# Kernel optimization log

Measured on AMD Instinct MI355X. Metric: run time of the kernel, lower is better.

Reference implementation:

```python
import jax, jax.numpy as jnp
import numpy as np

N = 50000      # nodes
E = 800000     # edges (before self-loops)
F_IN = 512     # input features
H = 8          # heads (layer 1)
C = 32         # hidden per head
CLS = 40       # classes


def setup_inputs() -> dict:
    key = jax.random.key(0)
    ks = jax.random.split(key, 10)
    small = lambda k, shape: jax.random.normal(k, shape, jnp.float32) * 0.05
    return {
        "x": jax.random.normal(ks[0], (N, F_IN), jnp.float32),
        "edge_index": jax.random.randint(ks[1], (2, E), 0, N, jnp.int32),
        # layer 1 params (GATConv: F_IN -> C per head, 8 heads, concat)
        "W1": small(ks[2], (F_IN, H * C)),
        "a_src1": small(ks[3], (H, C)),
        "a_dst1": small(ks[4], (H, C)),
        "b1": jnp.zeros((H * C,), jnp.float32),
        # layer 2 params (GATConv: H*C -> CLS, 1 head)
        "W2": small(ks[5], (H * C, CLS)),
        "a_src2": small(ks[6], (1, CLS)),
        "a_dst2": small(ks[7], (1, CLS)),
        "b2": jnp.zeros((CLS,), jnp.float32),
    }


def gat_conv(x, W, a_src, a_dst, b, src, dst, n):
    """PyG-style GATConv (negative_slope=0.2); self-loops already in src/dst."""
    h_, c_ = a_src.shape
    h = (x @ W).reshape(n, h_, c_)                       # [N, H, C]
    alpha_src = jnp.einsum('nhc,hc->nh', h, a_src)       # [N, H]
    alpha_dst = jnp.einsum('nhc,hc->nh', h, a_dst)       # [N, H]
    e = jax.nn.leaky_relu(alpha_src[src] + alpha_dst[dst], 0.2)  # [E', H]
    # segment softmax over incoming edges of each destination node
    m = jax.lax.stop_gradient(jax.ops.segment_max(e, dst, num_segments=n))
    ex = jnp.exp(e - m[dst])
    den = jax.ops.segment_sum(ex, dst, num_segments=n)
    alpha = ex / (den[dst] + 1e-16)                      # [E', H]
    out = jax.ops.segment_sum(h[src] * alpha[:, :, None], dst, num_segments=n)
    return out.reshape(n, h_ * c_) + b


def reference(x, edge_index, W1, a_src1, a_dst1, b1, W2, a_src2, a_dst2, b2):
    n = x.shape[0]
    loop = jnp.arange(n, dtype=edge_index.dtype)
    src = jnp.concatenate([edge_index[0], loop])  # add self-loops (PyG default)
    dst = jnp.concatenate([edge_index[1], loop])
    # dropout is identity at inference
    h = jax.nn.elu(gat_conv(x, W1, a_src1, a_dst1, b1, src, dst, n))
    out = gat_conv(h, W2, a_src2, a_dst2, b2, src, dst, n)
    return jax.nn.log_softmax(out, axis=1)
```

## Files before the change

kernel.cpp:

```cpp
#include <hip/hip_runtime.h>
#include <hip/hip_bf16.h>
#include <math.h>

constexpr int NN  = 50000;
constexpr int NE  = 800000;
constexpr int EP  = NE + NN;
constexpr int FIN = 512;
constexpr int NH  = 8;
constexpr int NC  = 32;
constexpr int HC  = NH * NC;
constexpr int CLS = 40;
constexpr int CLSP = 48;
constexpr int DSTR = 16;
constexpr int NGB  = (NN + 63) / 64;
constexpr int NHB  = (NE + 255) / 256;
constexpr int NFB  = NGB + NHB;
constexpr int NP2B = (EP + 255) / 256;
constexpr int CVTW_ITEMS = HC * (FIN / 8) + CLSP * HC;
constexpr int CVTW_B = (CVTW_ITEMS + 255) / 256;

typedef __attribute__((ext_vector_type(8))) __bf16 bf16x8;
typedef __attribute__((ext_vector_type(4))) __bf16 bf16x4;
typedef __attribute__((ext_vector_type(4))) float f32x4;
typedef __attribute__((ext_vector_type(2))) float f32x2;

__device__ inline bf16x8 cvt8v(const f32x4 a, const f32x4 b) {
  bf16x8 o;
  o[0] = (__bf16)a.x; o[1] = (__bf16)a.y; o[2] = (__bf16)a.z; o[3] = (__bf16)a.w;
  o[4] = (__bf16)b.x; o[5] = (__bf16)b.y; o[6] = (__bf16)b.z; o[7] = (__bf16)b.w;
  return o;
}

__device__ inline unsigned char to_fp8(float f) {
  int pk = __builtin_amdgcn_cvt_pk_fp8_f32(f, f, 0, false);
  return (unsigned char)(pk & 0xff);
}

__device__ inline float from_fp8(unsigned char b) {
  f32x2 v = __builtin_amdgcn_cvt_pk_f32_fp8((unsigned)b, false);
  return v.x;
}

__global__ void k_cvtw(const float* __restrict__ W1, const float* __restrict__ W2,
                       __bf16* __restrict__ Wt, __bf16* __restrict__ W2t) {
  int t = blockIdx.x * 256 + threadIdx.x;
  if (t < HC * (FIN / 8)) {
    int c = t >> 6, kq = (t & 63) * 8;
    bf16x8 o;
#pragma unroll
    for (int j = 0; j < 8; ++j) o[j] = (__bf16)W1[(size_t)(kq + j) * HC + c];
    *(bf16x8*)&Wt[(size_t)c * FIN + kq] = o;
  } else if (t < CVTW_ITEMS) {
    int u = t - HC * (FIN / 8);
    int c = u >> 8, k = u & 255;
    W2t[u] = (c < CLS) ? (__bf16)W2[(size_t)k * CLS + c] : (__bf16)0.f;
  }
}

__global__ __launch_bounds__(256) void k_gemm1_hist(
    const float* __restrict__ X, const __bf16* __restrict__ Wt,
    const float* __restrict__ a_s1, const float* __restrict__ a_d1,
    unsigned char* __restrict__ Hout, float* __restrict__ asrc1,
    float* __restrict__ adst1,
    const int* __restrict__ ei, int* __restrict__ degp,
    int* __restrict__ rank) {
  __shared__ __align__(16) float Xp[2][4096];
  const int tid = threadIdx.x;

  if (blockIdx.x >= NGB) {
    int e = (blockIdx.x - NGB) * 256 + tid;
    if (e < NE) {
      int d = ei[NE + e];
      rank[e] = atomicAdd(&degp[(size_t)d * DSTR], 1);
    }
    return;
  }

  const int lane = tid & 63;
  const int w    = tid >> 6;
  const int wn   = w * 64;
  const int bm   = blockIdx.x * 64;
  const int l15  = lane & 15, lg = lane >> 4;

  const int srow_l  = (lane >> 4);
  const int sslot   = (l15 >> 1);
  const int shalf   = (lane & 1);

  f32x4 acc[4][4] = {};

  auto issue = [&](int c, int buf) {
#pragma unroll
    for (int jj = 0; jj < 4; ++jj) {
      const int j = w * 4 + jj;
      const int row_l = 4 * j + srow_l;
      const int rowG = min(bm + row_l, NN - 1);
      const int g = sslot ^ (row_l & 7);
      const float* src = X + (size_t)rowG * FIN + c * 64 + g * 8 + shalf * 4;
      __builtin_amdgcn_global_load_lds(
          (const __attribute__((address_space(1))) void*)src,
          (__attribute__((address_space(3))) void*)(&Xp[buf][j * 256]), 16, 0, 0);
    }
  };

  issue(0, 0);
  for (int c = 0; c < 8; ++c) {
    const int cur = c & 1;
    __syncthreads();
    if (c < 7) issue(c + 1, cur ^ 1);

#pragma unroll
    for (int kh = 0; kh < 2; ++kh) {
      const int kb = lg + 4 * kh;
      bf16x8 bv[4];
#pragma unroll
      for (int ni = 0; ni < 4; ++ni)
        bv[ni] = *(const bf16x8*)(Wt + (size_t)(wn + ni * 16 + l15) * FIN
                                     + c * 64 + kb * 8);
#pragma unroll
      for (int mi = 0; mi < 4; ++mi) {
        int r = mi * 16 + l15;
        int fo = r * 64 + ((kb ^ (r & 7)) << 3);
        f32x4 alo = *(const f32x4*)&Xp[cur][fo];
        f32x4 ahi = *(const f32x4*)&Xp[cur][fo + 4];
        bf16x8 av = cvt8v(alo, ahi);
#pragma unroll
        for (int ni = 0; ni < 4; ++ni)
          acc[mi][ni] = __builtin_amdgcn_mfma_f32_16x16x32_bf16(
              av, bv[ni], acc[mi][ni], 0, 0, 0);
      }
    }
  }

  const int hbase = 2 * w;
#pragma unroll
  for (int hh = 0; hh < 2; ++hh) {
    float asA = a_s1[(hbase + hh) * NC + l15];
    float asB = a_s1[(hbase + hh) * NC + 16 + l15];
    float adA = a_d1[(hbase + hh) * NC + l15];
    float adB = a_d1[(hbase + hh) * NC + 16 + l15];
    float vs = 0.f, vd = 0.f;
#pragma unroll
    for (int mi = 0; mi < 4; ++mi) {
#pragma unroll
      for (int r = 0; r < 4; ++r) {
        float ps = acc[mi][2 * hh][r] * asA + acc[mi][2 * hh + 1][r] * asB;
        float pd = acc[mi][2 * hh][r] * adA + acc[mi][2 * hh + 1][r] * adB;
#pragma unroll
        for (int off = 1; off < 16; off <<= 1) {
          ps += __shfl_xor(ps, off, 64);
          pd += __shfl_xor(pd, off, 64);
        }
        if (l15 == mi * 4 + r) { vs = ps; vd = pd; }
      }
    }
    int rw = bm + (l15 >> 2) * 16 + lg * 4 + (l15 & 3);
    if (rw < NN) {
      asrc1[(size_t)rw * NH + hbase + hh] = vs;
      adst1[(size_t)rw * NH + hbase + hh] = vd;
    }
  }

#pragma unroll
  for (int mi = 0; mi < 4; ++mi) {
#pragma unroll
    for (int ni = 0; ni < 4; ++ni) {
      int col = wn + ni * 16 + l15;
#pragma unroll
      for (int r = 0; r < 4; ++r) {
        int row = bm + mi * 16 + lg * 4 + r;
        if (row < NN) Hout[(size_t)row * HC + col] = to_fp8(acc[mi][ni][r]);
      }
    }
  }
}

__global__ __launch_bounds__(1024) void k_scan1(const int* __restrict__ degp,
                                                int* __restrict__ rowptr1,
                                                int* __restrict__ bsum, int n) {
  __shared__ int sm[1024];
  int i = blockIdx.x * 1024 + threadIdx.x;
  int v = (i < n) ? degp[(size_t)i * DSTR] + 1 : 0;
  sm[threadIdx.x] = v;
  __syncthreads();
  for (int off = 1; off < 1024; off <<= 1) {
    int t = (threadIdx.x >= off) ? sm[threadIdx.x - off] : 0;
    __syncthreads();
    sm[threadIdx.x] += t;
    __syncthreads();
  }
  if (i < n) rowptr1[i] = sm[threadIdx.x];
  if (threadIdx.x == 1023) bsum[blockIdx.x] = sm[1023];
}

__global__ void k_scan23(int* __restrict__ rowptr, const int* __restrict__ bsum,
                         int nb, int n) {
  __shared__ int off[64];
  if (threadIdx.x < 64) {
    int lane = threadIdx.x;
    int v = (lane < nb) ? bsum[lane] : 0;
#pragma unroll
    for (int o = 1; o < 64; o <<= 1) {
      int t = __shfl_up(v, o);
      if (lane >= o) v += t;
    }
    int ex = __shfl_up(v, 1);
    if (lane == 0) ex = 0;
    off[lane] = ex;
  }
  __syncthreads();
  int i = blockIdx.x * 256 + threadIdx.x;
  if (i == 0) rowptr[0] = 0;
  if (i < n) rowptr[i + 1] += off[i >> 10];
}

__global__ void k_pass2(const int* __restrict__ ei, const int* __restrict__ rank,
                        const int* __restrict__ rowptr,
                        unsigned short* __restrict__ srcS) {
  int e = blockIdx.x * 256 + threadIdx.x;
  if (e >= EP) return;
  if (e < NE) {
    int s = ei[e], d = ei[NE + e];
    srcS[rowptr[d] + rank[e]] = (unsigned short)s;
  } else {
    int d = e - NE;
    srcS[rowptr[d + 1] - 1] = (unsigned short)d;
  }
}

__global__ __launch_bounds__(256) void k_agg1(const unsigned char* __restrict__ h1f8,
                                              const float* __restrict__ asrc,
                                              const float* __restrict__ adst,
                                              const unsigned short* __restrict__ srcS,
                                              const int* __restrict__ rowptr,
                                              const float* __restrict__ b1,
                                              __bf16* __restrict__ helu) {
  int wave = (blockIdx.x * 256 + threadIdx.x) >> 6;
  int lane = threadIdx.x & 63;
  if (wave >= NN) return;
  int lo = rowptr[wave], hi = rowptr[wave + 1];
  int head = lane >> 3;
  int hw   = lane & 7;
  float adstv = adst[wave * NH + head];
  float ad2   = adst[wave * NH + hw];
  float4 acc = {0.f, 0.f, 0.f, 0.f};
  float den = 0.f;

  for (int base = lo; base < hi; base += 64) {
    int cnt = hi - base; if (cnt > 64) cnt = 64;
    int sv = (lane < cnt) ? (int)srcS[base + lane] : 0;
    int j = 0;
    for (; j + 8 <= cnt; j += 8) {
      int se = __shfl(sv, j + head);
      float v = asrc[se * NH + hw] + ad2;
      v = v > 0.f ? v : 0.2f * v;
      float wv = __expf(v);
      int s[8]; unsigned int hv[8];
#pragma unroll
      for (int u = 0; u < 8; ++u) s[u] = __shfl(sv, j + u);
#pragma unroll
      for (int u = 0; u < 8; ++u)
        hv[u] = *(const unsigned int*)&h1f8[(size_t)s[u] * HC + lane * 4];
#pragma unroll
      for (int u = 0; u < 8; ++u) {
        float wu = __shfl(wv, u * 8 + head);
        f32x2 lo2 = __builtin_amdgcn_cvt_pk_f32_fp8(hv[u], false);
        f32x2 hi2 = __builtin_amdgcn_cvt_pk_f32_fp8(hv[u], true);
        acc.x += wu * lo2.x;
        acc.y += wu * lo2.y;
        acc.z += wu * hi2.x;
        acc.w += wu * hi2.y;
        den += wu;
      }
    }
    for (; j < cnt; ++j) {
      int s = __shfl(sv, j);
      float v = asrc[s * NH + head] + adstv;
      v = v > 0.f ? v : 0.2f * v;
      float w = __expf(v);
      unsigned int hv = *(const unsigned int*)&h1f8[(size_t)s * HC + lane * 4];
      f32x2 lo2 = __builtin_amdgcn_cvt_pk_f32_fp8(hv, false);
      f32x2 hi2 = __builtin_amdgcn_cvt_pk_f32_fp8(hv, true);
      acc.x += w * lo2.x;
      acc.y += w * lo2.y;
      acc.z += w * hi2.x;
      acc.w += w * hi2.y;
      den += w;
    }
  }

  float inv = 1.f / (den + 1e-16f);
  float4 bb = *(const float4*)&b1[lane * 4];
  float o[4] = {acc.x * inv + bb.x, acc.y * inv + bb.y,
                acc.z * inv + bb.z, acc.w * inv + bb.w};
  bf16x4 ov;
#pragma unroll
  for (int j2 = 0; j2 < 4; ++j2) {
    float e = o[j2] > 0.f ? o[j2] : expm1f(o[j2]);
    ov[j2] = (__bf16)e;
  }
  *(bf16x4*)&helu[(size_t)wave * HC + lane * 4] = ov;
}

__global__ __launch_bounds__(256) void k_gemm2m(const __bf16* __restrict__ A,
                                                const __bf16* __restrict__ W2t,
                                                const float* __restrict__ a_s2,
                                                const float* __restrict__ a_d2,
                                                unsigned char* __restrict__ h2p,
                                                float* __restrict__ asrc2,
                                                float* __restrict__ adst2) {
  __shared__ __align__(16) __bf16 As[128 * 8 * 8];
  __shared__ __align__(16) __bf16 Bsh[CLSP * 33 * 8];
  const int tid  = threadIdx.x;
  const int lane = tid & 63;
  const int w    = tid >> 6;
  const int wm   = w * 32;
  const int bm   = blockIdx.x * 128;

  const int l3 = lane >> 3;
  const int l7 = lane & 7;
  const int kb_src = l7 ^ l3;

  for (int s = tid; s < CLSP * 32; s += 256) {
    int c = s >> 5, kb = s & 31;
    *(bf16x8*)(Bsh + (size_t)(c * 33 + kb) * 8) =
        *(const bf16x8*)(W2t + (size_t)c * HC + kb * 8);
  }

  f32x4 acc[2][3] = {};

  for (int step = 0; step < 4; ++step) {
    const int k0 = step * 64;
#pragma unroll
    for (int q = 0; q < 4; ++q) {
      const int inst = w * 4 + q;
      const int r = inst * 8 + l3;
      const int arow = min(bm + r, NN - 1);
      const __bf16* ga = A + (size_t)arow * HC + k0 + kb_src * 8;
      __builtin_amdgcn_global_load_lds(
          (const __attribute__((address_space(1))) void*)ga,
          (__attribute__((address_space(3))) void*)(As + inst * 512), 16, 0, 0);
    }
    __syncthreads();

    const int l15 = lane & 15, lg = lane >> 4;
#pragma unroll
    for (int kh = 0; kh < 2; ++kh) {
      const int kbl = lg + 4 * kh;
      const int kbg = step * 8 + kbl;
      bf16x8 av[2], bv[3];
#pragma unroll
      for (int mi = 0; mi < 2; ++mi) {
        int r = wm + mi * 16 + l15;
        av[mi] = *(const bf16x8*)(As + (size_t)(r * 8 + (kbl ^ (r & 7))) * 8);
      }
#pragma unroll
      for (int ni = 0; ni < 3; ++ni) {
        int c = ni * 16 + l15;
        bv[ni] = *(const bf16x8*)(Bsh + (size_t)(c * 33 + kbg) * 8);
      }
#pragma unroll
      for (int mi = 0; mi < 2; ++mi)
#pragma unroll
        for (int ni = 0; ni < 3; ++ni)
          acc[mi][ni] = __builtin_amdgcn_mfma_f32_16x16x32_bf16(
              av[mi], bv[ni], acc[mi][ni], 0, 0, 0);
    }
    __syncthreads();
  }

  const int l15 = lane & 15, lg = lane >> 4;

  {
    int c0 = l15, c1 = 16 + l15, c2 = 32 + l15;
    float as0 = a_s2[c0], as1 = a_s2[c1], as2v = (c2 < CLS) ? a_s2[c2] : 0.f;
    float ad0 = a_d2[c0], ad1 = a_d2[c1], ad2v = (c2 < CLS) ? a_d2[c2] : 0.f;
    float vs = 0.f, vd = 0.f;
#pragma unroll
    for (int mi = 0; mi < 2; ++mi) {
#pragma unroll
      for (int r = 0; r < 4; ++r) {
        float ps = acc[mi][0][r] * as0 + acc[mi][1][r] * as1 + acc[mi][2][r] * as2v;
        float pd = acc[mi][0][r] * ad0 + acc[mi][1][r] * ad1 + acc[mi][2][r] * ad2v;
#pragma unroll
        for (int off = 1; off < 16; off <<= 1) {
          ps += __shfl_xor(ps, off, 64);
          pd += __shfl_xor(pd, off, 64);
        }
        if (l15 == mi * 4 + r) { vs = ps; vd = pd; }
      }
    }
    int rw = bm + wm + (l15 >> 2) * 16 + lg * 4 + (l15 & 3);
    if (l15 < 8 && rw < NN) {
      asrc2[rw] = vs;
      adst2[rw] = vd;
    }
  }

#pragma unroll
  for (int mi = 0; mi < 2; ++mi) {
#pragma unroll
    for (int ni = 0; ni < 3; ++ni) {
      int col = ni * 16 + l15;
      if (col >= CLS) continue;
#pragma unroll
      for (int r = 0; r < 4; ++r) {
        int row = bm + wm + mi * 16 + lg * 4 + r;
        if (row < NN) h2p[(size_t)row * 64 + col] = to_fp8(acc[mi][ni][r]);
      }
    }
  }
}

__global__ __launch_bounds__(256) void k_agg2(const unsigned char* __restrict__ h2p,
                                              const float* __restrict__ asrc,
                                              const float* __restrict__ adst,
                                              const unsigned short* __restrict__ srcS,
                                              const int* __restrict__ rowptr,
                                              const float* __restrict__ b2,
                                              float* __restrict__ out) {
  int wave = (blockIdx.x * 256 + threadIdx.x) >> 6;
  int lane = threadIdx.x & 63;
  if (wave >= NN) return;
  int lo = rowptr[wave], hi = rowptr[wave + 1];
  bool act = lane < CLS;
  float adstv = adst[wave];
  float acc = 0.f, den = 0.f;

  for (int base = lo; base < hi; base += 64) {
    int cnt = hi - base; if (cnt > 64) cnt = 64;
    int sv = (lane < cnt) ? (int)srcS[base + lane] : 0;
    float v = asrc[sv] + adstv;
    v = v > 0.f ? v : 0.2f * v;
    float wv = __expf(v);
    int j = 0;
    for (; j + 8 <= cnt; j += 8) {
      int s[8]; float hval[8];
#pragma unroll
      for (int u = 0; u < 8; ++u) s[u] = __shfl(sv, j + u);
#pragma unroll
      for (int u = 0; u < 8; ++u)
        hval[u] = act ? from_fp8(h2p[(size_t)s[u] * 64 + lane]) : 0.f;
#pragma unroll
      for (int u = 0; u < 8; ++u) {
        float wu = __shfl(wv, j + u);
        acc += wu * hval[u];
        den += wu;
      }
    }
    for (; j < cnt; ++j) {
      int s = __shfl(sv, j);
      float wu = __shfl(wv, j);
      if (act) acc += wu * from_fp8(h2p[(size_t)s * 64 + lane]);
      den += wu;
    }
  }

  float o = act ? (acc / (den + 1e-16f) + b2[lane]) : -INFINITY;
  float m = o;
#pragma unroll
  for (int off = 32; off; off >>= 1) m = fmaxf(m, __shfl_xor(m, off, 64));
  float ex = act ? __expf(o - m) : 0.f;
  float ssum = ex;
#pragma unroll
  for (int off = 32; off; off >>= 1) ssum += __shfl_xor(ssum, off, 64);
  if (act) out[(size_t)wave * CLS + lane] = o - m - logf(ssum);
}

extern "C" void kernel_launch(void* const* d_in, const int* in_sizes, int n_in,
                              void* d_out, int out_size, void* d_ws, size_t ws_size,
                              hipStream_t stream) {
  const float* x      = (const float*)d_in[0];
  const int*   ei     = (const int*)d_in[1];
  const float* W1     = (const float*)d_in[2];
  const float* a_src1 = (const float*)d_in[3];
  const float* a_dst1 = (const float*)d_in[4];
  const float* b1     = (const float*)d_in[5];
  const float* W2     = (const float*)d_in[6];
  const float* a_src2 = (const float*)d_in[7];
  const float* a_dst2 = (const float*)d_in[8];
  const float* b2     = (const float*)d_in[9];
  float* out = (float*)d_out;

  char* p = (char*)d_ws;
  auto alloc = [&](size_t bytes) {
    char* r = p;
    p += (bytes + 255) & ~size_t(255);
    return r;
  };
  unsigned char* h1f8 = (unsigned char*)alloc((size_t)NN * HC);
  __bf16* helu  = (__bf16*)alloc((size_t)NN * HC * 2);
  __bf16* Wt    = (__bf16*)alloc((size_t)HC * FIN * 2);
  __bf16* W2t   = (__bf16*)alloc((size_t)CLSP * HC * 2);
  unsigned char* h2p = (unsigned char*)alloc((size_t)NN * 64);
  float*  asrc1 = (float*)alloc((size_t)NN * NH * 4);
  float*  adst1 = (float*)alloc((size_t)NN * NH * 4);
  float*  asrc2 = (float*)alloc((size_t)NN * 4);
  float*  adst2 = (float*)alloc((size_t)NN * 4);
  unsigned short* srcS = (unsigned short*)alloc((size_t)EP * 2);
  int*    rank  = (int*)alloc((size_t)NE * 4);
  int*    degp  = (int*)alloc((size_t)NN * DSTR * 4);
  int*    rowptr= (int*)alloc((size_t)(NN + 1) * 4);
  int*    bsum  = (int*)alloc(256 * 4);

  const int nbScan = (NN + 1023) / 1024;

  hipMemsetAsync(degp, 0, (size_t)NN * DSTR * 4, stream);
  k_cvtw<<<CVTW_B, 256, 0, stream>>>(W1, W2, Wt, W2t);

  k_gemm1_hist<<<NFB, 256, 0, stream>>>(x, Wt, a_src1, a_dst1,
                                        h1f8, asrc1, adst1,
                                        ei, degp, rank);

  k_scan1<<<nbScan, 1024, 0, stream>>>(degp, rowptr + 1, bsum, NN);
  k_scan23<<<(NN + 255) / 256, 256, 0, stream>>>(rowptr, bsum, nbScan, NN);

  k_pass2<<<NP2B, 256, 0, stream>>>(ei, rank, rowptr, srcS);

  k_agg1<<<(NN + 3) / 4, 256, 0, stream>>>(h1f8, asrc1, adst1, srcS, rowptr, b1, helu);

  k_gemm2m<<<(NN + 127) / 128, 256, 0, stream>>>(helu, W2t, a_src2, a_dst2,
                                                 h2p, asrc2, adst2);

  k_agg2<<<(NN + 3) / 4, 256, 0, stream>>>(h2p, asrc2, adst2, srcS, rowptr, b2, out);
}
```

Before: 193.7 us.

## Load X tiles directly from global into registers, dropping LDS double buffer

The first GEMM no longer stages X through a double-buffered LDS tile filled by global_load_lds. Each wave now loads its X rows straight from global memory into registers, converts them to bf16, and feeds the MFMAs. This removes the per-chunk __syncthreads and the LDS traffic. In exchange, all four waves in a block now read the same X rows redundantly from global/L2, and there is no explicit prefetch overlap.

```diff
diff --git a/kernel.cpp b/kernel.cpp
--- a/kernel.cpp
+++ b/kernel.cpp
@@ -64,7 +64,6 @@
     float* __restrict__ adst1,
     const int* __restrict__ ei, int* __restrict__ degp,
     int* __restrict__ rank) {
-  __shared__ __align__(16) float Xp[2][4096];
   const int tid = threadIdx.x;
 
   if (blockIdx.x >= NGB) {
@@ -82,53 +81,43 @@
   const int bm   = blockIdx.x * 64;
   const int l15  = lane & 15, lg = lane >> 4;
 
-  const int srow_l  = (lane >> 4);
-  const int sslot   = (l15 >> 1);
-  const int shalf   = (lane & 1);
+  const float* xrow[4];
+#pragma unroll
+  for (int mi = 0; mi < 4; ++mi)
+    xrow[mi] = X + (size_t)min(bm + mi * 16 + l15, NN - 1) * FIN + lg * 8;
+  const __bf16* wrow[4];
+#pragma unroll
+  for (int ni = 0; ni < 4; ++ni)
+    wrow[ni] = Wt + (size_t)(wn + ni * 16 + l15) * FIN + lg * 8;
 
   f32x4 acc[4][4] = {};
 
-  auto issue = [&](int c, int buf) {
-#pragma unroll
-    for (int jj = 0; jj < 4; ++jj) {
-      const int j = w * 4 + jj;
-      const int row_l = 4 * j + srow_l;
-      const int rowG = min(bm + row_l, NN - 1);
-      const int g = sslot ^ (row_l & 7);
-      const float* src = X + (size_t)rowG * FIN + c * 64 + g * 8 + shalf * 4;
-      __builtin_amdgcn_global_load_lds(
-          (const __attribute__((address_space(1))) void*)src,
-          (__attribute__((address_space(3))) void*)(&Xp[buf][j * 256]), 16, 0, 0);
-    }
-  };
-
-  issue(0, 0);
   for (int c = 0; c < 8; ++c) {
-    const int cur = c & 1;
-    __syncthreads();
-    if (c < 7) issue(c + 1, cur ^ 1);
-
-#pragma unroll
-    for (int kh = 0; kh < 2; ++kh) {
-      const int kb = lg + 4 * kh;
-      bf16x8 bv[4];
-#pragma unroll
-      for (int ni = 0; ni < 4; ++ni)
-        bv[ni] = *(const bf16x8*)(Wt + (size_t)(wn + ni * 16 + l15) * FIN
-                                     + c * 64 + kb * 8);
-#pragma unroll
-      for (int mi = 0; mi < 4; ++mi) {
-        int r = mi * 16 + l15;
-        int fo = r * 64 + ((kb ^ (r & 7)) << 3);
-        f32x4 alo = *(const f32x4*)&Xp[cur][fo];
-        f32x4 ahi = *(const f32x4*)&Xp[cur][fo + 4];
-        bf16x8 av = cvt8v(alo, ahi);
-#pragma unroll
-        for (int ni = 0; ni < 4; ++ni)
-          acc[mi][ni] = __builtin_amdgcn_mfma_f32_16x16x32_bf16(
-              av, bv[ni], acc[mi][ni], 0, 0, 0);
-      }
-    }
+    const int k0 = c * 64;
+    bf16x8 av0[4], av1[4], bv0[4], bv1[4];
+#pragma unroll
+    for (int mi = 0; mi < 4; ++mi) {
+      f32x4 lo0 = *(const f32x4*)(xrow[mi] + k0);
+      f32x4 hi0 = *(const f32x4*)(xrow[mi] + k0 + 4);
+      f32x4 lo1 = *(const f32x4*)(xrow[mi] + k0 + 32);
+      f32x4 hi1 = *(const f32x4*)(xrow[mi] + k0 + 36);
+      av0[mi] = cvt8v(lo0, hi0);
+      av1[mi] = cvt8v(lo1, hi1);
+    }
+#pragma unroll
+    for (int ni = 0; ni < 4; ++ni) {
+      bv0[ni] = *(const bf16x8*)(wrow[ni] + k0);
+      bv1[ni] = *(const bf16x8*)(wrow[ni] + k0 + 32);
+    }
+#pragma unroll
+    for (int mi = 0; mi < 4; ++mi)
+#pragma unroll
+      for (int ni = 0; ni < 4; ++ni) {
+        acc[mi][ni] = __builtin_amdgcn_mfma_f32_16x16x32_bf16(
+            av0[mi], bv0[ni], acc[mi][ni], 0, 0, 0);
+        acc[mi][ni] = __builtin_amdgcn_mfma_f32_16x16x32_bf16(
+            av1[mi], bv1[ni], acc[mi][ni], 0, 0, 0);
+      }
   }
 
   const int hbase = 2 * w;
```

Measured after the change: 233.9 us. 1.21x slower.
